# Kernel tuning notes

Measured on AMD Instinct MI355X. Metric: run time of the kernel, lower is better.

The kernel has to match this reference:

```python
import jax, jax.numpy as jnp
import numpy as np

EPS = 1e-06


def euler_xyz_to_mat(e):
    # scipy Rotation.from_euler('xyz', [a,b,c]) is extrinsic: R = Rz(c) @ Ry(b) @ Rx(a)
    a, b, c = e[..., 0], e[..., 1], e[..., 2]
    sa, ca = jnp.sin(a), jnp.cos(a)
    sb, cb = jnp.sin(b), jnp.cos(b)
    sc, cc = jnp.sin(c), jnp.cos(c)
    r00 = cc * cb
    r01 = cc * sb * sa - sc * ca
    r02 = cc * sb * ca + sc * sa
    r10 = sc * cb
    r11 = sc * sb * sa + cc * ca
    r12 = sc * sb * ca - cc * sa
    r20 = -sb
    r21 = cb * sa
    r22 = cb * ca
    R = jnp.stack([r00, r01, r02, r10, r11, r12, r20, r21, r22], axis=-1)
    return R.reshape(e.shape[:-1] + (3, 3))


def to_transform(positions, orientations):
    # positions, orientations: [B, S, 3] -> poses [B, S, 4, 4]
    R = euler_xyz_to_mat(orientations)
    top = jnp.concatenate([R, positions[..., None]], axis=-1)  # [B,S,3,4]
    bottom = jnp.broadcast_to(
        jnp.array([0.0, 0.0, 0.0, 1.0], dtype=positions.dtype),
        positions.shape[:2] + (1, 4))
    return jnp.concatenate([top, bottom], axis=-2)


def odometry_to_track(poses):
    # cumulative left-product along seq: track[0]=I, track[i]=track[i-1] @ poses[:, i]
    B = poses.shape[0]
    eye = jnp.broadcast_to(jnp.eye(4, dtype=poses.dtype), (B, 1, 4, 4))
    shifted = jnp.concatenate([eye, poses[:, 1:]], axis=1)
    return jax.lax.associative_scan(
        lambda x, y: jnp.einsum('bsij,bsjk->bsik', x, y), shifted, axis=1)


def rotation_loss(rot1, rot2):
    # geodesic angle between rotations via trace of R1 @ R2^T
    R = jnp.einsum('bsij,bskj->bsik', rot1, rot2)
    cos = (R[:, :, 0, 0] + R[:, :, 1, 1] + R[:, :, 2, 2] - 1.0) / 2.0
    cos = jnp.clip(cos, -1.0 + EPS, 1.0 - EPS)
    return jnp.mean(jnp.arccos(cos))


def setup_inputs() -> dict:
    key = jax.random.key(0)
    k1, k2, k3 = jax.random.split(key, 3)
    B, S = 64, 4096
    return {
        'y_hat': jax.random.normal(k1, (B, S, 6), dtype=jnp.float32),
        'gt_positions': jax.random.normal(k2, (B, S, 3), dtype=jnp.float32),
        'gt_orientations': jax.random.normal(k3, (B, S, 3), dtype=jnp.float32),
    }


def reference(y_hat, gt_positions, gt_orientations):
    alphas = (1.0, 1.0)
    betas = (1.0, 1.0)
    gammas = (0.5, 0.5)

    pred_ori = y_hat[:, :, :3]
    pred_pos = y_hat[:, :, 3:]

    # ---- odometry loss ----
    mse_pos = jnp.mean((pred_pos - gt_positions) ** 2)
    mae_pos = jnp.mean(jnp.abs(pred_pos - gt_positions))
    pose_est = to_transform(pred_pos, pred_ori)
    pose_gt = to_transform(gt_positions, gt_orientations)
    odom_rot = rotation_loss(pose_est[:, :, :3, :3], pose_gt[:, :, :3, :3])
    odom_loss = alphas[0] * odom_rot + alphas[1] * (mse_pos + mae_pos)

    # ---- trajectory loss ----
    traj_gt = odometry_to_track(pose_gt)
    traj_est = odometry_to_track(pose_est)
    t_gt = traj_gt[:, :, :3, 3]
    t_est = traj_est[:, :, :3, 3]
    traj_mse = jnp.mean((t_est - t_gt) ** 2)
    traj_mae = jnp.mean(jnp.abs(t_est - t_gt))
    traj_rot = rotation_loss(traj_est[:, :, :3, :3], traj_gt[:, :, :3, :3])
    traj_loss = betas[0] * traj_rot + betas[1] * (traj_mse + traj_mae)

    return gammas[0] * odom_loss + gammas[1] * traj_loss
```

## Files before the change

### kernel.cpp

```cpp
#include <hip/hip_runtime.h>
#include <math.h>

#define NB 64
#define NS 4096
#define SEGS 8
#define TPB 256
#define CHUNK 2
#define STEPS (NS / SEGS)
#define NWAVES (TPB / 64)
#define NSEGB (NB * SEGS)
#define K3_TPB 512
#define K3_W (K3_TPB / 64)
#define FTPB 512

#define FB_T 512
#define FB_CHUNK (NS / FB_T)
#define FB_W (FB_T / 64)

struct SE3 {
  float r[9];
  float t[3];
};

__device__ __forceinline__ void se3_id(SE3 &x) {
#pragma unroll
  for (int i = 0; i < 9; ++i) x.r[i] = 0.f;
  x.r[0] = x.r[4] = x.r[8] = 1.f;
  x.t[0] = x.t[1] = x.t[2] = 0.f;
}

__device__ __forceinline__ SE3 se3_mul(const SE3 &a, const SE3 &b) {
  SE3 c;
#pragma unroll
  for (int i = 0; i < 3; ++i) {
#pragma unroll
    for (int j = 0; j < 3; ++j) {
      c.r[i * 3 + j] = fmaf(a.r[i * 3 + 0], b.r[0 * 3 + j],
                       fmaf(a.r[i * 3 + 1], b.r[1 * 3 + j],
                            a.r[i * 3 + 2] * b.r[2 * 3 + j]));
    }
    c.t[i] = fmaf(a.r[i * 3 + 0], b.t[0],
             fmaf(a.r[i * 3 + 1], b.t[1],
             fmaf(a.r[i * 3 + 2], b.t[2], a.t[i])));
  }
  return c;
}

__device__ __forceinline__ float fast_acosf(float x) {
  const float ax = fabsf(x);
  float p = fmaf(ax, -0.0187293f, 0.0742610f);
  p = fmaf(p, ax, -0.2121144f);
  p = fmaf(p, ax, 1.5707288f);
  const float r = sqrtf(fmaxf(1.f - ax, 0.f)) * p;
  return (x >= 0.f) ? r : (3.14159274f - r);
}

__device__ __forceinline__ float clip_acos_from_trace(float tr) {
  float cosv = 0.5f * (tr - 1.f);
  cosv = fminf(fmaxf(cosv, -1.f + 1e-6f), 1.f - 1e-6f);
  return fast_acosf(cosv);
}

__device__ __forceinline__ SE3 build_pose(float a, float b, float c,
                                          float tx, float ty, float tz) {
  float sa, ca, sb, cb, sc, cc;
  __sincosf(a, &sa, &ca);
  __sincosf(b, &sb, &cb);
  __sincosf(c, &sc, &cc);
  SE3 p;
  p.r[0] = cc * cb;
  p.r[1] = cc * sb * sa - sc * ca;
  p.r[2] = cc * sb * ca + sc * sa;
  p.r[3] = sc * cb;
  p.r[4] = sc * sb * sa + cc * ca;
  p.r[5] = sc * sb * ca - cc * sa;
  p.r[6] = -sb;
  p.r[7] = cb * sa;
  p.r[8] = cb * ca;
  p.t[0] = tx;
  p.t[1] = ty;
  p.t[2] = tz;
  return p;
}

__device__ __forceinline__ SE3 se3_shfl_up(const SE3 &x, int delta) {
  SE3 y;
#pragma unroll
  for (int i = 0; i < 9; ++i) y.r[i] = __shfl_up(x.r[i], delta, 64);
#pragma unroll
  for (int i = 0; i < 3; ++i) y.t[i] = __shfl_up(x.t[i], delta, 64);
  return y;
}

__device__ __forceinline__ float geo_angle(const SE3 &A, const SE3 &B) {
  float dot = 0.f;
#pragma unroll
  for (int k = 0; k < 9; ++k) dot = fmaf(A.r[k], B.r[k], dot);
  return clip_acos_from_trace(dot);
}


__device__ __forceinline__ void step_store(float4 *base, const SE3 &Le,
                                           const SE3 &Lg, int s) {
  float m[9];
#pragma unroll
  for (int i = 0; i < 3; ++i)
#pragma unroll
    for (int j = 0; j < 3; ++j)
      m[i * 3 + j] = fmaf(Le.r[i * 3 + 0], Lg.r[j * 3 + 0],
                     fmaf(Le.r[i * 3 + 1], Lg.r[j * 3 + 1],
                          Le.r[i * 3 + 2] * Lg.r[j * 3 + 2]));
  base[0 * NS + s] = make_float4(m[0], m[1], m[2], m[3]);
  base[1 * NS + s] = make_float4(m[4], m[5], m[6], m[7]);
  base[2 * NS + s] = make_float4(m[8], Le.t[0], Le.t[1], Le.t[2]);
  base[3 * NS + s] = make_float4(Lg.t[0], Lg.t[1], Lg.t[2], 0.f);
}

__device__ __forceinline__ void block_reduce3_store(float v0, float v1,
                                                    float v2,
                                                    float *__restrict__ dst,
                                                    int lane, int wave,
                                                    int tid, int nwaves) {
#pragma unroll
  for (int o = 32; o > 0; o >>= 1) {
    v0 += __shfl_xor(v0, o, 64);
    v1 += __shfl_xor(v1, o, 64);
    v2 += __shfl_xor(v2, o, 64);
  }
  __shared__ float red[8][3];
  if (lane == 0) {
    red[wave][0] = v0;
    red[wave][1] = v1;
    red[wave][2] = v2;
  }
  __syncthreads();
  if (tid == 0) {
    float a = 0.f, b = 0.f, c = 0.f;
    for (int w = 0; w < nwaves; ++w) {
      a += red[w][0];
      b += red[w][1];
      c += red[w][2];
    }
    dst[0] = a;
    dst[1] = b;
    dst[2] = c;
  }
}

__global__ __launch_bounds__(TPB) void k1_scan(
    const float *__restrict__ y_hat, const float *__restrict__ gt_pos,
    const float *__restrict__ gt_ori, float *__restrict__ wsl,
    float *__restrict__ aggs, float *__restrict__ part1) {
  const int blk = blockIdx.x;
  const int b = blk >> 3;
  const int seg = blk & (SEGS - 1);
  const int tid = threadIdx.x;
  const int lane = tid & 63;
  const int wave = tid >> 6;
  const int s0 = seg * STEPS + tid * CHUNK;

  float s_sq = 0.f, s_abs = 0.f, s_rot = 0.f;

  SE3 P1e, P1g, P2e, P2g;
  {
    const float *y6 = y_hat + ((size_t)b * NS + s0) * 6;
    const float *g3 = gt_pos + ((size_t)b * NS + s0) * 3;
    const float *o3 = gt_ori + ((size_t)b * NS + s0) * 3;
    const float px = y6[3], py = y6[4], pz = y6[5];
    const float gx = g3[0], gy = g3[1], gz = g3[2];
    P1e = build_pose(y6[0], y6[1], y6[2], px, py, pz);
    P1g = build_pose(o3[0], o3[1], o3[2], gx, gy, gz);
    const float dx = px - gx, dy = py - gy, dz = pz - gz;
    s_sq += dx * dx + dy * dy + dz * dz;
    s_abs += fabsf(dx) + fabsf(dy) + fabsf(dz);
    s_rot += geo_angle(P1e, P1g);
    if (s0 == 0) {
      se3_id(P1e);
      se3_id(P1g);
    }
  }
  {
    const int s1 = s0 + 1;
    const float *y6 = y_hat + ((size_t)b * NS + s1) * 6;
    const float *g3 = gt_pos + ((size_t)b * NS + s1) * 3;
    const float *o3 = gt_ori + ((size_t)b * NS + s1) * 3;
    const float px = y6[3], py = y6[4], pz = y6[5];
    const float gx = g3[0], gy = g3[1], gz = g3[2];
    P2e = build_pose(y6[0], y6[1], y6[2], px, py, pz);
    P2g = build_pose(o3[0], o3[1], o3[2], gx, gy, gz);
    const float dx = px - gx, dy = py - gy, dz = pz - gz;
    s_sq += dx * dx + dy * dy + dz * dz;
    s_abs += fabsf(dx) + fabsf(dy) + fabsf(dz);
    s_rot += geo_angle(P2e, P2g);
  }

  SE3 Ie = se3_mul(P1e, P2e);
  SE3 Ig = se3_mul(P1g, P2g);
#pragma unroll
  for (int o = 1; o < 64; o <<= 1) {
    SE3 pe = se3_shfl_up(Ie, o);
    SE3 pg = se3_shfl_up(Ig, o);
    if (lane >= o) {
      Ie = se3_mul(pe, Ie);
      Ig = se3_mul(pg, Ig);
    }
  }

  SE3 Ee = se3_shfl_up(Ie, 1);
  SE3 Eg = se3_shfl_up(Ig, 1);
  if (lane == 0) {
    se3_id(Ee);
    se3_id(Eg);
  }

  __shared__ float aggE[NWAVES][12];
  __shared__ float aggG[NWAVES][12];
  if (lane == 63) {
#pragma unroll
    for (int k = 0; k < 9; ++k) {
      aggE[wave][k] = Ie.r[k];
      aggG[wave][k] = Ig.r[k];
    }
#pragma unroll
    for (int k = 0; k < 3; ++k) {
      aggE[wave][9 + k] = Ie.t[k];
      aggG[wave][9 + k] = Ig.t[k];
    }
  }
  __syncthreads();

  SE3 We, Wg;
  se3_id(We);
  se3_id(Wg);
  for (int w = 0; w < wave; ++w) {
    SE3 ae, ag;
#pragma unroll
    for (int k = 0; k < 9; ++k) {
      ae.r[k] = aggE[w][k];
      ag.r[k] = aggG[w][k];
    }
#pragma unroll
    for (int k = 0; k < 3; ++k) {
      ae.t[k] = aggE[w][9 + k];
      ag.t[k] = aggG[w][9 + k];
    }
    We = se3_mul(We, ae);
    Wg = se3_mul(Wg, ag);
  }

  SE3 Be = se3_mul(We, Ee);
  SE3 Bg = se3_mul(Wg, Eg);

  SE3 L1e = se3_mul(Be, P1e);
  SE3 L1g = se3_mul(Bg, P1g);
  SE3 L2e = se3_mul(L1e, P2e);
  SE3 L2g = se3_mul(L1g, P2g);

  float4 *wb4 = (float4 *)(wsl + (size_t)b * 16 * NS);
  step_store(wb4, L1e, L1g, s0);
  step_store(wb4, L2e, L2g, s0 + 1);

  if (tid == TPB - 1) {
    float *ag = aggs + (size_t)blk * 24;
#pragma unroll
    for (int k = 0; k < 9; ++k) {
      ag[k] = L2e.r[k];
      ag[12 + k] = L2g.r[k];
    }
#pragma unroll
    for (int k = 0; k < 3; ++k) {
      ag[9 + k] = L2e.t[k];
      ag[21 + k] = L2g.t[k];
    }
  }

  block_reduce3_store(s_sq, s_abs, s_rot, part1 + (size_t)blk * 3, lane, wave,
                      tid, NWAVES);
}

__global__ __launch_bounds__(K3_TPB) void k3_traj(const float *__restrict__ wsl,
                                                  const float *__restrict__ aggs,
                                                  float *__restrict__ part2) {
  const int blk = blockIdx.x;
  const int b = blk >> 3;
  const int seg = blk & (SEGS - 1);
  const int tid = threadIdx.x;
  const int lane = tid & 63;
  const int wave = tid >> 6;
  const int s = seg * STEPS + tid;

  SE3 Ee, Eg;
  se3_id(Ee);
  se3_id(Eg);
  const float *abase = aggs + (size_t)(b * SEGS) * 24;
  for (int w = 0; w < seg; ++w) {
    const float *ag = abase + (size_t)w * 24;
    SE3 ae, agm;
#pragma unroll
    for (int k = 0; k < 9; ++k) {
      ae.r[k] = ag[k];
      agm.r[k] = ag[12 + k];
    }
#pragma unroll
    for (int k = 0; k < 3; ++k) {
      ae.t[k] = ag[9 + k];
      agm.t[k] = ag[21 + k];
    }
    Ee = se3_mul(Ee, ae);
    Eg = se3_mul(Eg, agm);
  }

  float G[9];
#pragma unroll
  for (int j = 0; j < 3; ++j)
#pragma unroll
    for (int k = 0; k < 3; ++k)
      G[j * 3 + k] = fmaf(Ee.r[0 * 3 + j], Eg.r[0 * 3 + k],
                     fmaf(Ee.r[1 * 3 + j], Eg.r[1 * 3 + k],
                          Ee.r[2 * 3 + j] * Eg.r[2 * 3 + k]));
  const float dt0x = Ee.t[0] - Eg.t[0];
  const float dt0y = Ee.t[1] - Eg.t[1];
  const float dt0z = Ee.t[2] - Eg.t[2];

  const float4 *wb4 = (const float4 *)(wsl + (size_t)b * 16 * NS);
  const float4 q0 = wb4[0 * NS + s];
  const float4 q1 = wb4[1 * NS + s];
  const float4 q2 = wb4[2 * NS + s];
  const float4 q3 = wb4[3 * NS + s];
  const float m[9] = {q0.x, q0.y, q0.z, q0.w, q1.x, q1.y, q1.z, q1.w, q2.x};
  const float ltx = q2.y, lty = q2.z, ltz = q2.w;
  const float gtx = q3.x, gty = q3.y, gtz = q3.z;

  float tr = 0.f;
#pragma unroll
  for (int k = 0; k < 9; ++k) tr = fmaf(m[k], G[k], tr);
  float s_rot = clip_acos_from_trace(tr);

  const float ux = fmaf(Ee.r[0], ltx, fmaf(Ee.r[1], lty, Ee.r[2] * ltz));
  const float uy = fmaf(Ee.r[3], ltx, fmaf(Ee.r[4], lty, Ee.r[5] * ltz));
  const float uz = fmaf(Ee.r[6], ltx, fmaf(Ee.r[7], lty, Ee.r[8] * ltz));
  const float vx = fmaf(Eg.r[0], gtx, fmaf(Eg.r[1], gty, Eg.r[2] * gtz));
  const float vy = fmaf(Eg.r[3], gtx, fmaf(Eg.r[4], gty, Eg.r[5] * gtz));
  const float vz = fmaf(Eg.r[6], gtx, fmaf(Eg.r[7], gty, Eg.r[8] * gtz));
  const float dx = ux - vx + dt0x;
  const float dy = uy - vy + dt0y;
  const float dz = uz - vz + dt0z;

  float s_sq = dx * dx + dy * dy + dz * dz;
  float s_abs = fabsf(dx) + fabsf(dy) + fabsf(dz);

  block_reduce3_store(s_sq, s_abs, s_rot, part2 + (size_t)blk * 3, lane, wave,
                      tid, K3_W);
}

__global__ __launch_bounds__(FTPB) void finalize_parts(
    const float *__restrict__ part1, const float *__restrict__ part2,
    float *__restrict__ out) {
  const int tid = threadIdx.x;
  const int lane = tid & 63;
  const int wave = tid >> 6;

  float v[6];
#pragma unroll
  for (int k = 0; k < 3; ++k) {
    v[k] = part1[(size_t)tid * 3 + k];
    v[3 + k] = part2[(size_t)tid * 3 + k];
  }
#pragma unroll
  for (int o = 32; o > 0; o >>= 1) {
#pragma unroll
    for (int k = 0; k < 6; ++k) v[k] += __shfl_xor(v[k], o, 64);
  }
  __shared__ float red[FTPB / 64][6];
  if (lane == 0) {
#pragma unroll
    for (int k = 0; k < 6; ++k) red[wave][k] = v[k];
  }
  __syncthreads();
  if (tid == 0) {
    double a[6];
#pragma unroll
    for (int k = 0; k < 6; ++k) {
      double t = 0.0;
#pragma unroll
      for (int w = 0; w < FTPB / 64; ++w) t += (double)red[w][k];
      a[k] = t;
    }
    const double n3 = (double)NB * (double)NS * 3.0;
    const double n1 = (double)NB * (double)NS;
    const double odom = a[2] / n1 + (a[0] / n3 + a[1] / n3);
    const double traj = a[5] / n1 + (a[3] / n3 + a[4] / n3);
    out[0] = (float)(0.5 * odom + 0.5 * traj);
  }
}

__global__ __launch_bounds__(FB_T) void traj_loss_main(
    const float *__restrict__ y_hat, const float *__restrict__ gt_pos,
    const float *__restrict__ gt_ori, double *__restrict__ acc) {
  const int b = blockIdx.x;
  const int tid = threadIdx.x;
  const int lane = tid & 63;
  const int wave = tid >> 6;
  const int s0 = tid * FB_CHUNK;

  const float *yb = y_hat + (size_t)b * NS * 6;
  const float *gp = gt_pos + (size_t)b * NS * 3;
  const float *go = gt_ori + (size_t)b * NS * 3;

  float s_sq_pos = 0.f, s_abs_pos = 0.f, s_rot_odom = 0.f;

  SE3 Le, Lg;
  se3_id(Le);
  se3_id(Lg);

  for (int i = 0; i < FB_CHUNK; ++i) {
    const int s = s0 + i;
    const float *y6 = yb + (size_t)s * 6;
    const float *g3 = gp + (size_t)s * 3;
    const float *o3 = go + (size_t)s * 3;
    const float px = y6[3], py = y6[4], pz = y6[5];
    const float gx = g3[0], gy = g3[1], gz = g3[2];

    SE3 Pe = build_pose(y6[0], y6[1], y6[2], px, py, pz);
    SE3 Pg = build_pose(o3[0], o3[1], o3[2], gx, gy, gz);

    const float dx = px - gx, dy = py - gy, dz = pz - gz;
    s_sq_pos += dx * dx + dy * dy + dz * dz;
    s_abs_pos += fabsf(dx) + fabsf(dy) + fabsf(dz);
    s_rot_odom += geo_angle(Pe, Pg);

    if (s != 0) {
      Le = se3_mul(Le, Pe);
      Lg = se3_mul(Lg, Pg);
    }
  }

  SE3 Ie = Le, Ig = Lg;
#pragma unroll
  for (int o = 1; o < 64; o <<= 1) {
    SE3 pe = se3_shfl_up(Ie, o);
    SE3 pg = se3_shfl_up(Ig, o);
    if (lane >= o) {
      Ie = se3_mul(pe, Ie);
      Ig = se3_mul(pg, Ig);
    }
  }

  __shared__ float aggE[FB_W][12];
  __shared__ float aggG[FB_W][12];
  if (lane == 63) {
#pragma unroll
    for (int k = 0; k < 9; ++k) {
      aggE[wave][k] = Ie.r[k];
      aggG[wave][k] = Ig.r[k];
    }
#pragma unroll
    for (int k = 0; k < 3; ++k) {
      aggE[wave][9 + k] = Ie.t[k];
      aggG[wave][9 + k] = Ig.t[k];
    }
  }
  __syncthreads();

  SE3 Te, Tg;
  se3_id(Te);
  se3_id(Tg);
  for (int w = 0; w < wave; ++w) {
    SE3 ae, ag;
#pragma unroll
    for (int k = 0; k < 9; ++k) {
      ae.r[k] = aggE[w][k];
      ag.r[k] = aggG[w][k];
    }
#pragma unroll
    for (int k = 0; k < 3; ++k) {
      ae.t[k] = aggE[w][9 + k];
      ag.t[k] = aggG[w][9 + k];
    }
    Te = se3_mul(Te, ae);
    Tg = se3_mul(Tg, ag);
  }

  SE3 Ee = se3_shfl_up(Ie, 1);
  SE3 Eg = se3_shfl_up(Ig, 1);
  if (lane == 0) {
    se3_id(Ee);
    se3_id(Eg);
  }
  Te = se3_mul(Te, Ee);
  Tg = se3_mul(Tg, Eg);

  float s_sq_tr = 0.f, s_abs_tr = 0.f, s_rot_tr = 0.f;
  for (int i = 0; i < FB_CHUNK; ++i) {
    const int s = s0 + i;
    const float *y6 = yb + (size_t)s * 6;
    const float *g3 = gp + (size_t)s * 3;
    const float *o3 = go + (size_t)s * 3;
    if (s != 0) {
      SE3 Pe = build_pose(y6[0], y6[1], y6[2], y6[3], y6[4], y6[5]);
      SE3 Pg = build_pose(o3[0], o3[1], o3[2], g3[0], g3[1], g3[2]);
      Te = se3_mul(Te, Pe);
      Tg = se3_mul(Tg, Pg);
    }
    const float dx = Te.t[0] - Tg.t[0];
    const float dy = Te.t[1] - Tg.t[1];
    const float dz = Te.t[2] - Tg.t[2];
    s_sq_tr += dx * dx + dy * dy + dz * dz;
    s_abs_tr += fabsf(dx) + fabsf(dy) + fabsf(dz);
    s_rot_tr += geo_angle(Te, Tg);
  }

#pragma unroll
  for (int o = 32; o > 0; o >>= 1) {
    s_sq_pos += __shfl_xor(s_sq_pos, o, 64);
    s_abs_pos += __shfl_xor(s_abs_pos, o, 64);
    s_rot_odom += __shfl_xor(s_rot_odom, o, 64);
    s_sq_tr += __shfl_xor(s_sq_tr, o, 64);
    s_abs_tr += __shfl_xor(s_abs_tr, o, 64);
    s_rot_tr += __shfl_xor(s_rot_tr, o, 64);
  }
  if (lane == 0) {
    atomicAdd(&acc[0], (double)s_sq_pos);
    atomicAdd(&acc[1], (double)s_abs_pos);
    atomicAdd(&acc[2], (double)s_rot_odom);
    atomicAdd(&acc[3], (double)s_sq_tr);
    atomicAdd(&acc[4], (double)s_abs_tr);
    atomicAdd(&acc[5], (double)s_rot_tr);
  }
}

__global__ void init_acc(double *acc) {
  const int i = threadIdx.x;
  if (i < 6) acc[i] = 0.0;
}

__global__ void finalize_acc(const double *__restrict__ acc,
                             float *__restrict__ out) {
  const double n3 = (double)NB * (double)NS * 3.0;
  const double n1 = (double)NB * (double)NS;
  const double odom = acc[2] / n1 + (acc[0] / n3 + acc[1] / n3);
  const double traj = acc[5] / n1 + (acc[3] / n3 + acc[4] / n3);
  out[0] = (float)(0.5 * odom + 0.5 * traj);
}

extern "C" void kernel_launch(void *const *d_in, const int *in_sizes, int n_in,
                              void *d_out, int out_size, void *d_ws,
                              size_t ws_size, hipStream_t stream) {
  const float *y_hat = (const float *)d_in[0];
  const float *gt_pos = (const float *)d_in[1];
  const float *gt_ori = (const float *)d_in[2];

  float *wsl = (float *)d_ws;
  const size_t wsl_elems = (size_t)NB * 16 * NS;
  float *aggs = wsl + wsl_elems;
  float *part1 = aggs + (size_t)NSEGB * 24;
  float *part2 = part1 + (size_t)NSEGB * 3;
  const size_t need = (wsl_elems + (size_t)NSEGB * 30) * sizeof(float);

  if (ws_size >= need) {
    k1_scan<<<NSEGB, TPB, 0, stream>>>(y_hat, gt_pos, gt_ori, wsl, aggs,
                                       part1);
    k3_traj<<<NSEGB, K3_TPB, 0, stream>>>(wsl, aggs, part2);
    finalize_parts<<<1, FTPB, 0, stream>>>(part1, part2, (float *)d_out);
  } else {
    double *acc = (double *)d_ws;
    init_acc<<<1, 64, 0, stream>>>(acc);
    traj_loss_main<<<NB, FB_T, 0, stream>>>(y_hat, gt_pos, gt_ori, acc);
    finalize_acc<<<1, 1, 0, stream>>>(acc, (float *)d_out);
  }
}
```

Before: 26.68 us.

## Represent rotations as unit quaternions in scan and trajectory kernels

```diff
diff --git a/kernel.cpp b/kernel.cpp
--- a/kernel.cpp
+++ b/kernel.cpp
@@ -17,33 +17,69 @@
 #define FB_CHUNK (NS / FB_T)
 #define FB_W (FB_T / 64)
 
-struct SE3 {
-  float r[9];
-  float t[3];
+struct Q {
+  float w, x, y, z;
 };
-
-__device__ __forceinline__ void se3_id(SE3 &x) {
-#pragma unroll
-  for (int i = 0; i < 9; ++i) x.r[i] = 0.f;
-  x.r[0] = x.r[4] = x.r[8] = 1.f;
-  x.t[0] = x.t[1] = x.t[2] = 0.f;
-}
-
-__device__ __forceinline__ SE3 se3_mul(const SE3 &a, const SE3 &b) {
-  SE3 c;
-#pragma unroll
-  for (int i = 0; i < 3; ++i) {
-#pragma unroll
-    for (int j = 0; j < 3; ++j) {
-      c.r[i * 3 + j] = fmaf(a.r[i * 3 + 0], b.r[0 * 3 + j],
-                       fmaf(a.r[i * 3 + 1], b.r[1 * 3 + j],
-                            a.r[i * 3 + 2] * b.r[2 * 3 + j]));
-    }
-    c.t[i] = fmaf(a.r[i * 3 + 0], b.t[0],
-             fmaf(a.r[i * 3 + 1], b.t[1],
-             fmaf(a.r[i * 3 + 2], b.t[2], a.t[i])));
-  }
+struct QT {
+  Q q;
+  float tx, ty, tz;
+};
+
+__device__ __forceinline__ Q qmul(const Q &a, const Q &b) {
+  Q c;
+  c.w = a.w * b.w - a.x * b.x - a.y * b.y - a.z * b.z;
+  c.x = a.w * b.x + b.w * a.x + a.y * b.z - a.z * b.y;
+  c.y = a.w * b.y + b.w * a.y + a.z * b.x - a.x * b.z;
+  c.z = a.w * b.z + b.w * a.z + a.x * b.y - a.y * b.x;
   return c;
+}
+
+__device__ __forceinline__ Q qconj(const Q &q) {
+  Q c;
+  c.w = q.w;
+  c.x = -q.x;
+  c.y = -q.y;
+  c.z = -q.z;
+  return c;
+}
+
+__device__ __forceinline__ void qrot(const Q &q, float vx, float vy, float vz,
+                                     float &ox, float &oy, float &oz) {
+  const float tx = 2.f * (q.y * vz - q.z * vy);
+  const float ty = 2.f * (q.z * vx - q.x * vz);
+  const float tz = 2.f * (q.x * vy - q.y * vx);
+  ox = vx + q.w * tx + (q.y * tz - q.z * ty);
+  oy = vy + q.w * ty + (q.z * tx - q.x * tz);
+  oz = vz + q.w * tz + (q.x * ty - q.y * tx);
+}
+
+__device__ __forceinline__ void qt_id(QT &x) {
+  x.q.w = 1.f;
+  x.q.x = x.q.y = x.q.z = 0.f;
+  x.tx = x.ty = x.tz = 0.f;
+}
+
+__device__ __forceinline__ QT qt_mul(const QT &a, const QT &b) {
+  QT c;
+  c.q = qmul(a.q, b.q);
+  float rx, ry, rz;
+  qrot(a.q, b.tx, b.ty, b.tz, rx, ry, rz);
+  c.tx = rx + a.tx;
+  c.ty = ry + a.ty;
+  c.tz = rz + a.tz;
+  return c;
+}
+
+__device__ __forceinline__ QT qt_shfl_up(const QT &v, int delta) {
+  QT y;
+  y.q.w = __shfl_up(v.q.w, delta, 64);
+  y.q.x = __shfl_up(v.q.x, delta, 64);
+  y.q.y = __shfl_up(v.q.y, delta, 64);
+  y.q.z = __shfl_up(v.q.z, delta, 64);
+  y.tx = __shfl_up(v.tx, delta, 64);
+  y.ty = __shfl_up(v.ty, delta, 64);
+  y.tz = __shfl_up(v.tz, delta, 64);
+  return y;
 }
 
 __device__ __forceinline__ float fast_acosf(float x) {
@@ -55,10 +91,319 @@
   return (x >= 0.f) ? r : (3.14159274f - r);
 }
 
-__device__ __forceinline__ float clip_acos_from_trace(float tr) {
-  float cosv = 0.5f * (tr - 1.f);
+__device__ __forceinline__ float angle_from_cos(float cosv) {
   cosv = fminf(fmaxf(cosv, -1.f + 1e-6f), 1.f - 1e-6f);
   return fast_acosf(cosv);
+}
+
+__device__ __forceinline__ Q euler_to_quat(float a, float b, float c) {
+  float sa, ca, sb, cb, sc, cc;
+  __sincosf(0.5f * a, &sa, &ca);
+  __sincosf(0.5f * b, &sb, &cb);
+  __sincosf(0.5f * c, &sc, &cc);
+  Q q;
+  q.w = cc * cb * ca + sc * sb * sa;
+  q.x = cc * cb * sa - sc * sb * ca;
+  q.y = cc * sb * ca + sc * cb * sa;
+  q.z = sc * cb * ca - cc * sb * sa;
+  return q;
+}
+
+__device__ __forceinline__ void block_reduce3_store(float v0, float v1,
+                                                    float v2,
+                                                    float *__restrict__ dst,
+                                                    int lane, int wave,
+                                                    int tid, int nwaves) {
+#pragma unroll
+  for (int o = 32; o > 0; o >>= 1) {
+    v0 += __shfl_xor(v0, o, 64);
+    v1 += __shfl_xor(v1, o, 64);
+    v2 += __shfl_xor(v2, o, 64);
+  }
+  __shared__ float red[8][3];
+  if (lane == 0) {
+    red[wave][0] = v0;
+    red[wave][1] = v1;
+    red[wave][2] = v2;
+  }
+  __syncthreads();
+  if (tid == 0) {
+    float a = 0.f, b = 0.f, c = 0.f;
+    for (int w = 0; w < nwaves; ++w) {
+      a += red[w][0];
+      b += red[w][1];
+      c += red[w][2];
+    }
+    dst[0] = a;
+    dst[1] = b;
+    dst[2] = c;
+  }
+}
+
+
+__global__ __launch_bounds__(TPB) void k1_scan(
+    const float *__restrict__ y_hat, const float *__restrict__ gt_pos,
+    const float *__restrict__ gt_ori, float *__restrict__ wsl,
+    float *__restrict__ aggs, float *__restrict__ part1) {
+  const int blk = blockIdx.x;
+  const int b = blk >> 3;
+  const int seg = blk & (SEGS - 1);
+  const int tid = threadIdx.x;
+  const int lane = tid & 63;
+  const int wave = tid >> 6;
+  const int s0 = seg * STEPS + tid * CHUNK;
+
+  float s_sq = 0.f, s_abs = 0.f, s_rot = 0.f;
+
+  QT P1e, P1g, P2e, P2g;
+  {
+    const float *y6 = y_hat + ((size_t)b * NS + s0) * 6;
+    const float *g3 = gt_pos + ((size_t)b * NS + s0) * 3;
+    const float *o3 = gt_ori + ((size_t)b * NS + s0) * 3;
+    const float px = y6[3], py = y6[4], pz = y6[5];
+    const float gx = g3[0], gy = g3[1], gz = g3[2];
+    P1e.q = euler_to_quat(y6[0], y6[1], y6[2]);
+    P1e.tx = px; P1e.ty = py; P1e.tz = pz;
+    P1g.q = euler_to_quat(o3[0], o3[1], o3[2]);
+    P1g.tx = gx; P1g.ty = gy; P1g.tz = gz;
+    const float dx = px - gx, dy = py - gy, dz = pz - gz;
+    s_sq += dx * dx + dy * dy + dz * dz;
+    s_abs += fabsf(dx) + fabsf(dy) + fabsf(dz);
+    const float d = P1e.q.w * P1g.q.w + P1e.q.x * P1g.q.x +
+                    P1e.q.y * P1g.q.y + P1e.q.z * P1g.q.z;
+    s_rot += angle_from_cos(2.f * d * d - 1.f);
+    if (s0 == 0) {
+      qt_id(P1e);
+      qt_id(P1g);
+    }
+  }
+  {
+    const int s1 = s0 + 1;
+    const float *y6 = y_hat + ((size_t)b * NS + s1) * 6;
+    const float *g3 = gt_pos + ((size_t)b * NS + s1) * 3;
+    const float *o3 = gt_ori + ((size_t)b * NS + s1) * 3;
+    const float px = y6[3], py = y6[4], pz = y6[5];
+    const float gx = g3[0], gy = g3[1], gz = g3[2];
+    P2e.q = euler_to_quat(y6[0], y6[1], y6[2]);
+    P2e.tx = px; P2e.ty = py; P2e.tz = pz;
+    P2g.q = euler_to_quat(o3[0], o3[1], o3[2]);
+    P2g.tx = gx; P2g.ty = gy; P2g.tz = gz;
+    const float dx = px - gx, dy = py - gy, dz = pz - gz;
+    s_sq += dx * dx + dy * dy + dz * dz;
+    s_abs += fabsf(dx) + fabsf(dy) + fabsf(dz);
+    const float d = P2e.q.w * P2g.q.w + P2e.q.x * P2g.q.x +
+                    P2e.q.y * P2g.q.y + P2e.q.z * P2g.q.z;
+    s_rot += angle_from_cos(2.f * d * d - 1.f);
+  }
+
+  QT Ie = qt_mul(P1e, P2e);
+  QT Ig = qt_mul(P1g, P2g);
+#pragma unroll
+  for (int o = 1; o < 64; o <<= 1) {
+    QT pe = qt_shfl_up(Ie, o);
+    QT pg = qt_shfl_up(Ig, o);
+    if (lane >= o) {
+      Ie = qt_mul(pe, Ie);
+      Ig = qt_mul(pg, Ig);
+    }
+  }
+
+  QT Ee = qt_shfl_up(Ie, 1);
+  QT Eg = qt_shfl_up(Ig, 1);
+  if (lane == 0) {
+    qt_id(Ee);
+    qt_id(Eg);
+  }
+
+  __shared__ float aggE[NWAVES][8];
+  __shared__ float aggG[NWAVES][8];
+  if (lane == 63) {
+    aggE[wave][0] = Ie.q.w; aggE[wave][1] = Ie.q.x;
+    aggE[wave][2] = Ie.q.y; aggE[wave][3] = Ie.q.z;
+    aggE[wave][4] = Ie.tx; aggE[wave][5] = Ie.ty; aggE[wave][6] = Ie.tz;
+    aggG[wave][0] = Ig.q.w; aggG[wave][1] = Ig.q.x;
+    aggG[wave][2] = Ig.q.y; aggG[wave][3] = Ig.q.z;
+    aggG[wave][4] = Ig.tx; aggG[wave][5] = Ig.ty; aggG[wave][6] = Ig.tz;
+  }
+  __syncthreads();
+
+  QT We, Wg;
+  qt_id(We);
+  qt_id(Wg);
+  for (int w = 0; w < wave; ++w) {
+    QT ae, ag;
+    ae.q.w = aggE[w][0]; ae.q.x = aggE[w][1];
+    ae.q.y = aggE[w][2]; ae.q.z = aggE[w][3];
+    ae.tx = aggE[w][4]; ae.ty = aggE[w][5]; ae.tz = aggE[w][6];
+    ag.q.w = aggG[w][0]; ag.q.x = aggG[w][1];
+    ag.q.y = aggG[w][2]; ag.q.z = aggG[w][3];
+    ag.tx = aggG[w][4]; ag.ty = aggG[w][5]; ag.tz = aggG[w][6];
+    We = qt_mul(We, ae);
+    Wg = qt_mul(Wg, ag);
+  }
+
+  QT Be = qt_mul(We, Ee);
+  QT Bg = qt_mul(Wg, Eg);
+
+  QT L1e = qt_mul(Be, P1e);
+  QT L1g = qt_mul(Bg, P1g);
+  QT L2e = qt_mul(L1e, P2e);
+  QT L2g = qt_mul(L1g, P2g);
+
+  float4 *q4 = (float4 *)(wsl + (size_t)b * 10 * NS);
+  float4 *lt4 = q4 + NS;
+  float2 *g2 = (float2 *)(lt4 + NS);
+  {
+    const Q qm = qmul(L1e.q, qconj(L1g.q));
+    q4[s0] = make_float4(qm.w, qm.x, qm.y, qm.z);
+    lt4[s0] = make_float4(L1e.tx, L1e.ty, L1e.tz, L1g.tx);
+    g2[s0] = make_float2(L1g.ty, L1g.tz);
+  }
+  {
+    const Q qm = qmul(L2e.q, qconj(L2g.q));
+    q4[s0 + 1] = make_float4(qm.w, qm.x, qm.y, qm.z);
+    lt4[s0 + 1] = make_float4(L2e.tx, L2e.ty, L2e.tz, L2g.tx);
+    g2[s0 + 1] = make_float2(L2g.ty, L2g.tz);
+  }
+
+  if (tid == TPB - 1) {
+    float *ag = aggs + (size_t)blk * 16;
+    ag[0] = L2e.q.w; ag[1] = L2e.q.x; ag[2] = L2e.q.y; ag[3] = L2e.q.z;
+    ag[4] = L2e.tx; ag[5] = L2e.ty; ag[6] = L2e.tz;
+    ag[8] = L2g.q.w; ag[9] = L2g.q.x; ag[10] = L2g.q.y; ag[11] = L2g.q.z;
+    ag[12] = L2g.tx; ag[13] = L2g.ty; ag[14] = L2g.tz;
+  }
+
+  block_reduce3_store(s_sq, s_abs, s_rot, part1 + (size_t)blk * 3, lane, wave,
+                      tid, NWAVES);
+}
+
+__global__ __launch_bounds__(K3_TPB) void k3_traj(const float *__restrict__ wsl,
+                                                  const float *__restrict__ aggs,
+                                                  float *__restrict__ part2) {
+  const int blk = blockIdx.x;
+  const int b = blk >> 3;
+  const int seg = blk & (SEGS - 1);
+  const int tid = threadIdx.x;
+  const int lane = tid & 63;
+  const int wave = tid >> 6;
+  const int s = seg * STEPS + tid;
+
+  QT Ee, Eg;
+  qt_id(Ee);
+  qt_id(Eg);
+  const float *abase = aggs + (size_t)(b * SEGS) * 16;
+  for (int w = 0; w < seg; ++w) {
+    const float *ag = abase + (size_t)w * 16;
+    QT ae, agm;
+    ae.q.w = ag[0]; ae.q.x = ag[1]; ae.q.y = ag[2]; ae.q.z = ag[3];
+    ae.tx = ag[4]; ae.ty = ag[5]; ae.tz = ag[6];
+    agm.q.w = ag[8]; agm.q.x = ag[9]; agm.q.y = ag[10]; agm.q.z = ag[11];
+    agm.tx = ag[12]; agm.ty = ag[13]; agm.tz = ag[14];
+    Ee = qt_mul(Ee, ae);
+    Eg = qt_mul(Eg, agm);
+  }
+
+  const Q u = qmul(qconj(Eg.q), Ee.q);
+  const float dt0x = Ee.tx - Eg.tx;
+  const float dt0y = Ee.ty - Eg.ty;
+  const float dt0z = Ee.tz - Eg.tz;
+
+  const float4 *q4 = (const float4 *)(wsl + (size_t)b * 10 * NS);
+  const float4 *lt4 = q4 + NS;
+  const float2 *g2 = (const float2 *)(lt4 + NS);
+  const float4 qm = q4[s];
+  const float4 lt = lt4[s];
+  const float2 gv = g2[s];
+
+  const float wdot = u.w * qm.x - u.x * qm.y - u.y * qm.z - u.z * qm.w;
+  (void)wdot;
+  const float mw = qm.x, mx = qm.y, my = qm.z, mz = qm.w;
+  const float wd = u.w * mw - u.x * mx - u.y * my - u.z * mz;
+  float s_rot = angle_from_cos(2.f * wd * wd - 1.f);
+
+  float ux, uy, uz, vx, vy, vz;
+  qrot(Ee.q, lt.x, lt.y, lt.z, ux, uy, uz);
+  qrot(Eg.q, lt.w, gv.x, gv.y, vx, vy, vz);
+  const float dx = ux - vx + dt0x;
+  const float dy = uy - vy + dt0y;
+  const float dz = uz - vz + dt0z;
+
+  float s_sq = dx * dx + dy * dy + dz * dz;
+  float s_abs = fabsf(dx) + fabsf(dy) + fabsf(dz);
+
+  block_reduce3_store(s_sq, s_abs, s_rot, part2 + (size_t)blk * 3, lane, wave,
+                      tid, K3_W);
+}
+
+__global__ __launch_bounds__(FTPB) void finalize_parts(
+    const float *__restrict__ part1, const float *__restrict__ part2,
+    float *__restrict__ out) {
+  const int tid = threadIdx.x;
+  const int lane = tid & 63;
+  const int wave = tid >> 6;
+
+  float v[6];
+#pragma unroll
+  for (int k = 0; k < 3; ++k) {
+    v[k] = part1[(size_t)tid * 3 + k];
+    v[3 + k] = part2[(size_t)tid * 3 + k];
+  }
+#pragma unroll
+  for (int o = 32; o > 0; o >>= 1) {
+#pragma unroll
+    for (int k = 0; k < 6; ++k) v[k] += __shfl_xor(v[k], o, 64);
+  }
+  __shared__ float red[FTPB / 64][6];
+  if (lane == 0) {
+#pragma unroll
+    for (int k = 0; k < 6; ++k) red[wave][k] = v[k];
+  }
+  __syncthreads();
+  if (tid == 0) {
+    double a[6];
+#pragma unroll
+    for (int k = 0; k < 6; ++k) {
+      double t = 0.0;
+#pragma unroll
+      for (int w = 0; w < FTPB / 64; ++w) t += (double)red[w][k];
+      a[k] = t;
+    }
+    const double n3 = (double)NB * (double)NS * 3.0;
+    const double n1 = (double)NB * (double)NS;
+    const double odom = a[2] / n1 + (a[0] / n3 + a[1] / n3);
+    const double traj = a[5] / n1 + (a[3] / n3 + a[4] / n3);
+    out[0] = (float)(0.5 * odom + 0.5 * traj);
+  }
+}
+
+struct SE3 {
+  float r[9];
+  float t[3];
+};
+
+__device__ __forceinline__ void se3_id(SE3 &x) {
+#pragma unroll
+  for (int i = 0; i < 9; ++i) x.r[i] = 0.f;
+  x.r[0] = x.r[4] = x.r[8] = 1.f;
+  x.t[0] = x.t[1] = x.t[2] = 0.f;
+}
+
+__device__ __forceinline__ SE3 se3_mul(const SE3 &a, const SE3 &b) {
+  SE3 c;
+#pragma unroll
+  for (int i = 0; i < 3; ++i) {
+#pragma unroll
+    for (int j = 0; j < 3; ++j) {
+      c.r[i * 3 + j] = fmaf(a.r[i * 3 + 0], b.r[0 * 3 + j],
+                       fmaf(a.r[i * 3 + 1], b.r[1 * 3 + j],
+                            a.r[i * 3 + 2] * b.r[2 * 3 + j]));
+    }
+    c.t[i] = fmaf(a.r[i * 3 + 0], b.t[0],
+             fmaf(a.r[i * 3 + 1], b.t[1],
+             fmaf(a.r[i * 3 + 2], b.t[2], a.t[i])));
+  }
+  return c;
 }
 
 __device__ __forceinline__ SE3 build_pose(float a, float b, float c,
@@ -96,302 +441,7 @@
   float dot = 0.f;
 #pragma unroll
   for (int k = 0; k < 9; ++k) dot = fmaf(A.r[k], B.r[k], dot);
-  return clip_acos_from_trace(dot);
-}
-
-
-__device__ __forceinline__ void step_store(float4 *base, const SE3 &Le,
-                                           const SE3 &Lg, int s) {
-  float m[9];
-#pragma unroll
-  for (int i = 0; i < 3; ++i)
-#pragma unroll
-    for (int j = 0; j < 3; ++j)
-      m[i * 3 + j] = fmaf(Le.r[i * 3 + 0], Lg.r[j * 3 + 0],
-                     fmaf(Le.r[i * 3 + 1], Lg.r[j * 3 + 1],
-                          Le.r[i * 3 + 2] * Lg.r[j * 3 + 2]));
-  base[0 * NS + s] = make_float4(m[0], m[1], m[2], m[3]);
-  base[1 * NS + s] = make_float4(m[4], m[5], m[6], m[7]);
-  base[2 * NS + s] = make_float4(m[8], Le.t[0], Le.t[1], Le.t[2]);
-  base[3 * NS + s] = make_float4(Lg.t[0], Lg.t[1], Lg.t[2], 0.f);
-}
-
-__device__ __forceinline__ void block_reduce3_store(float v0, float v1,
-                                                    float v2,
-                                                    float *__restrict__ dst,
-                                                    int lane, int wave,
-                                                    int tid, int nwaves) {
-#pragma unroll
-  for (int o = 32; o > 0; o >>= 1) {
-    v0 += __shfl_xor(v0, o, 64);
-    v1 += __shfl_xor(v1, o, 64);
-    v2 += __shfl_xor(v2, o, 64);
-  }
-  __shared__ float red[8][3];
-  if (lane == 0) {
-    red[wave][0] = v0;
-    red[wave][1] = v1;
-    red[wave][2] = v2;
-  }
-  __syncthreads();
-  if (tid == 0) {
-    float a = 0.f, b = 0.f, c = 0.f;
-    for (int w = 0; w < nwaves; ++w) {
-      a += red[w][0];
-      b += red[w][1];
-      c += red[w][2];
-    }
-    dst[0] = a;
-    dst[1] = b;
-    dst[2] = c;
-  }
-}
-
-__global__ __launch_bounds__(TPB) void k1_scan(
-    const float *__restrict__ y_hat, const float *__restrict__ gt_pos,
-    const float *__restrict__ gt_ori, float *__restrict__ wsl,
-    float *__restrict__ aggs, float *__restrict__ part1) {
-  const int blk = blockIdx.x;
-  const int b = blk >> 3;
-  const int seg = blk & (SEGS - 1);
-  const int tid = threadIdx.x;
-  const int lane = tid & 63;
-  const int wave = tid >> 6;
-  const int s0 = seg * STEPS + tid * CHUNK;
-
-  float s_sq = 0.f, s_abs = 0.f, s_rot = 0.f;
-
-  SE3 P1e, P1g, P2e, P2g;
-  {
-    const float *y6 = y_hat + ((size_t)b * NS + s0) * 6;
-    const float *g3 = gt_pos + ((size_t)b * NS + s0) * 3;
-    const float *o3 = gt_ori + ((size_t)b * NS + s0) * 3;
-    const float px = y6[3], py = y6[4], pz = y6[5];
-    const float gx = g3[0], gy = g3[1], gz = g3[2];
-    P1e = build_pose(y6[0], y6[1], y6[2], px, py, pz);
-    P1g = build_pose(o3[0], o3[1], o3[2], gx, gy, gz);
-    const float dx = px - gx, dy = py - gy, dz = pz - gz;
-    s_sq += dx * dx + dy * dy + dz * dz;
-    s_abs += fabsf(dx) + fabsf(dy) + fabsf(dz);
-    s_rot += geo_angle(P1e, P1g);
-    if (s0 == 0) {
-      se3_id(P1e);
-      se3_id(P1g);
-    }
-  }
-  {
-    const int s1 = s0 + 1;
-    const float *y6 = y_hat + ((size_t)b * NS + s1) * 6;
-    const float *g3 = gt_pos + ((size_t)b * NS + s1) * 3;
-    const float *o3 = gt_ori + ((size_t)b * NS + s1) * 3;
-    const float px = y6[3], py = y6[4], pz = y6[5];
-    const float gx = g3[0], gy = g3[1], gz = g3[2];
-    P2e = build_pose(y6[0], y6[1], y6[2], px, py, pz);
-    P2g = build_pose(o3[0], o3[1], o3[2], gx, gy, gz);
-    const float dx = px - gx, dy = py - gy, dz = pz - gz;
-    s_sq += dx * dx + dy * dy + dz * dz;
-    s_abs += fabsf(dx) + fabsf(dy) + fabsf(dz);
-    s_rot += geo_angle(P2e, P2g);
-  }
-
-  SE3 Ie = se3_mul(P1e, P2e);
-  SE3 Ig = se3_mul(P1g, P2g);
-#pragma unroll
-  for (int o = 1; o < 64; o <<= 1) {
-    SE3 pe = se3_shfl_up(Ie, o);
-    SE3 pg = se3_shfl_up(Ig, o);
-    if (lane >= o) {
-      Ie = se3_mul(pe, Ie);
-      Ig = se3_mul(pg, Ig);
-    }
-  }
-
-  SE3 Ee = se3_shfl_up(Ie, 1);
-  SE3 Eg = se3_shfl_up(Ig, 1);
-  if (lane == 0) {
-    se3_id(Ee);
-    se3_id(Eg);
-  }
-
-  __shared__ float aggE[NWAVES][12];
-  __shared__ float aggG[NWAVES][12];
-  if (lane == 63) {
-#pragma unroll
-    for (int k = 0; k < 9; ++k) {
-      aggE[wave][k] = Ie.r[k];
-      aggG[wave][k] = Ig.r[k];
-    }
-#pragma unroll
-    for (int k = 0; k < 3; ++k) {
-      aggE[wave][9 + k] = Ie.t[k];
-      aggG[wave][9 + k] = Ig.t[k];
-    }
-  }
-  __syncthreads();
-
-  SE3 We, Wg;
-  se3_id(We);
-  se3_id(Wg);
-  for (int w = 0; w < wave; ++w) {
-    SE3 ae, ag;
-#pragma unroll
-    for (int k = 0; k < 9; ++k) {
-      ae.r[k] = aggE[w][k];
-      ag.r[k] = aggG[w][k];
-    }
-#pragma unroll
-    for (int k = 0; k < 3; ++k) {
-      ae.t[k] = aggE[w][9 + k];
-      ag.t[k] = aggG[w][9 + k];
-    }
-    We = se3_mul(We, ae);
-    Wg = se3_mul(Wg, ag);
-  }
-
-  SE3 Be = se3_mul(We, Ee);
-  SE3 Bg = se3_mul(Wg, Eg);
-
-  SE3 L1e = se3_mul(Be, P1e);
-  SE3 L1g = se3_mul(Bg, P1g);
-  SE3 L2e = se3_mul(L1e, P2e);
-  SE3 L2g = se3_mul(L1g, P2g);
-
-  float4 *wb4 = (float4 *)(wsl + (size_t)b * 16 * NS);
-  step_store(wb4, L1e, L1g, s0);
-  step_store(wb4, L2e, L2g, s0 + 1);
-
-  if (tid == TPB - 1) {
-    float *ag = aggs + (size_t)blk * 24;
-#pragma unroll
-    for (int k = 0; k < 9; ++k) {
-      ag[k] = L2e.r[k];
-      ag[12 + k] = L2g.r[k];
-    }
-#pragma unroll
-    for (int k = 0; k < 3; ++k) {
-      ag[9 + k] = L2e.t[k];
-      ag[21 + k] = L2g.t[k];
-    }
-  }
-
-  block_reduce3_store(s_sq, s_abs, s_rot, part1 + (size_t)blk * 3, lane, wave,
-                      tid, NWAVES);
-}
-
-__global__ __launch_bounds__(K3_TPB) void k3_traj(const float *__restrict__ wsl,
-                                                  const float *__restrict__ aggs,
-                                                  float *__restrict__ part2) {
-  const int blk = blockIdx.x;
-  const int b = blk >> 3;
-  const int seg = blk & (SEGS - 1);
-  const int tid = threadIdx.x;
-  const int lane = tid & 63;
-  const int wave = tid >> 6;
-  const int s = seg * STEPS + tid;
-
-  SE3 Ee, Eg;
-  se3_id(Ee);
-  se3_id(Eg);
-  const float *abase = aggs + (size_t)(b * SEGS) * 24;
-  for (int w = 0; w < seg; ++w) {
-    const float *ag = abase + (size_t)w * 24;
-    SE3 ae, agm;
-#pragma unroll
-    for (int k = 0; k < 9; ++k) {
-      ae.r[k] = ag[k];
-      agm.r[k] = ag[12 + k];
-    }
-#pragma unroll
-    for (int k = 0; k < 3; ++k) {
-      ae.t[k] = ag[9 + k];
-      agm.t[k] = ag[21 + k];
-    }
-    Ee = se3_mul(Ee, ae);
-    Eg = se3_mul(Eg, agm);
-  }
-
-  float G[9];
-#pragma unroll
-  for (int j = 0; j < 3; ++j)
-#pragma unroll
-    for (int k = 0; k < 3; ++k)
-      G[j * 3 + k] = fmaf(Ee.r[0 * 3 + j], Eg.r[0 * 3 + k],
-                     fmaf(Ee.r[1 * 3 + j], Eg.r[1 * 3 + k],
-                          Ee.r[2 * 3 + j] * Eg.r[2 * 3 + k]));
-  const float dt0x = Ee.t[0] - Eg.t[0];
-  const float dt0y = Ee.t[1] - Eg.t[1];
-  const float dt0z = Ee.t[2] - Eg.t[2];
-
-  const float4 *wb4 = (const float4 *)(wsl + (size_t)b * 16 * NS);
-  const float4 q0 = wb4[0 * NS + s];
-  const float4 q1 = wb4[1 * NS + s];
-  const float4 q2 = wb4[2 * NS + s];
-  const float4 q3 = wb4[3 * NS + s];
-  const float m[9] = {q0.x, q0.y, q0.z, q0.w, q1.x, q1.y, q1.z, q1.w, q2.x};
-  const float ltx = q2.y, lty = q2.z, ltz = q2.w;
-  const float gtx = q3.x, gty = q3.y, gtz = q3.z;
-
-  float tr = 0.f;
-#pragma unroll
-  for (int k = 0; k < 9; ++k) tr = fmaf(m[k], G[k], tr);
-  float s_rot = clip_acos_from_trace(tr);
-
-  const float ux = fmaf(Ee.r[0], ltx, fmaf(Ee.r[1], lty, Ee.r[2] * ltz));
-  const float uy = fmaf(Ee.r[3], ltx, fmaf(Ee.r[4], lty, Ee.r[5] * ltz));
-  const float uz = fmaf(Ee.r[6], ltx, fmaf(Ee.r[7], lty, Ee.r[8] * ltz));
-  const float vx = fmaf(Eg.r[0], gtx, fmaf(Eg.r[1], gty, Eg.r[2] * gtz));
-  const float vy = fmaf(Eg.r[3], gtx, fmaf(Eg.r[4], gty, Eg.r[5] * gtz));
-  const float vz = fmaf(Eg.r[6], gtx, fmaf(Eg.r[7], gty, Eg.r[8] * gtz));
-  const float dx = ux - vx + dt0x;
-  const float dy = uy - vy + dt0y;
-  const float dz = uz - vz + dt0z;
-
-  float s_sq = dx * dx + dy * dy + dz * dz;
-  float s_abs = fabsf(dx) + fabsf(dy) + fabsf(dz);
-
-  block_reduce3_store(s_sq, s_abs, s_rot, part2 + (size_t)blk * 3, lane, wave,
-                      tid, K3_W);
-}
-
-__global__ __launch_bounds__(FTPB) void finalize_parts(
-    const float *__restrict__ part1, const float *__restrict__ part2,
-    float *__restrict__ out) {
-  const int tid = threadIdx.x;
-  const int lane = tid & 63;
-  const int wave = tid >> 6;
-
-  float v[6];
-#pragma unroll
-  for (int k = 0; k < 3; ++k) {
-    v[k] = part1[(size_t)tid * 3 + k];
-    v[3 + k] = part2[(size_t)tid * 3 + k];
-  }
-#pragma unroll
-  for (int o = 32; o > 0; o >>= 1) {
-#pragma unroll
-    for (int k = 0; k < 6; ++k) v[k] += __shfl_xor(v[k], o, 64);
-  }
-  __shared__ float red[FTPB / 64][6];
-  if (lane == 0) {
-#pragma unroll
-    for (int k = 0; k < 6; ++k) red[wave][k] = v[k];
-  }
-  __syncthreads();
-  if (tid == 0) {
-    double a[6];
-#pragma unroll
-    for (int k = 0; k < 6; ++k) {
-      double t = 0.0;
-#pragma unroll
-      for (int w = 0; w < FTPB / 64; ++w) t += (double)red[w][k];
-      a[k] = t;
-    }
-    const double n3 = (double)NB * (double)NS * 3.0;
-    const double n1 = (double)NB * (double)NS;
-    const double odom = a[2] / n1 + (a[0] / n3 + a[1] / n3);
-    const double traj = a[5] / n1 + (a[3] / n3 + a[4] / n3);
-    out[0] = (float)(0.5 * odom + 0.5 * traj);
-  }
+  return angle_from_cos(0.5f * (dot - 1.f));
 }
 
 __global__ __launch_bounds__(FB_T) void traj_loss_main(
@@ -551,11 +601,11 @@
   const float *gt_ori = (const float *)d_in[2];
 
   float *wsl = (float *)d_ws;
-  const size_t wsl_elems = (size_t)NB * 16 * NS;
+  const size_t wsl_elems = (size_t)NB * 10 * NS;
   float *aggs = wsl + wsl_elems;
-  float *part1 = aggs + (size_t)NSEGB * 24;
+  float *part1 = aggs + (size_t)NSEGB * 16;
   float *part2 = part1 + (size_t)NSEGB * 3;
-  const size_t need = (wsl_elems + (size_t)NSEGB * 30) * sizeof(float);
+  const size_t need = (wsl_elems + (size_t)NSEGB * 22) * sizeof(float);
 
   if (ws_size >= need) {
     k1_scan<<<NSEGB, TPB, 0, stream>>>(y_hat, gt_pos, gt_ori, wsl, aggs,
```

After: 24.73 us. -7.3%, faster.
